# Performance work log

Hardware: AMD Instinct MI355X
Metric: run time of the kernel (lower is better)

## Reference

```python
import jax, jax.numpy as jnp
import numpy as np

CHUNK = 128
EPS = 1e-12


def causal_prod(q, k, v, chunk=CHUNK):
    """Chunk-parallel causal linear attention numerator and denominator.
    q,k: [B,H,S,D]; v: [B,H,S,E].
    Returns N: [B,H,S,E] = q_n . cumsum_{m<=n}(k_m v_m^T)
            D: [B,H,S]   = q_n . cumsum_{m<=n} k_m
    """
    B, H, S, D = q.shape
    E = v.shape[-1]
    nc = S // chunk
    # [nc, B, H, C, D]
    qc = q.reshape(B, H, nc, chunk, D).transpose(2, 0, 1, 3, 4)
    kc = k.reshape(B, H, nc, chunk, D).transpose(2, 0, 1, 3, 4)
    vc = v.reshape(B, H, nc, chunk, E).transpose(2, 0, 1, 3, 4)
    mask = jnp.tril(jnp.ones((chunk, chunk), dtype=bool))  # j <= i

    def step(carry, xs):
        S_state, Z_state = carry  # [B,H,D,E], [B,H,D]
        qb, kb, vb = xs           # [B,H,C,D], [B,H,C,D], [B,H,C,E]
        scores = jnp.einsum('bhid,bhjd->bhij', qb, kb)
        scores = jnp.where(mask, scores, 0.0)
        # intra-chunk causal part + inter-chunk state part
        Nb = jnp.einsum('bhij,bhje->bhie', scores, vb) \
             + jnp.einsum('bhid,bhde->bhie', qb, S_state)
        Db = scores.sum(-1) + jnp.einsum('bhid,bhd->bhi', qb, Z_state)
        S_state = S_state + jnp.einsum('bhjd,bhje->bhde', kb, vb)
        Z_state = Z_state + kb.sum(axis=2)
        return (S_state, Z_state), (Nb, Db)

    init = (jnp.zeros((B, H, D, E), q.dtype), jnp.zeros((B, H, D), q.dtype))
    _, (N, Dv) = jax.lax.scan(step, init, (qc, kc, vc))
    N = N.transpose(1, 2, 0, 3, 4).reshape(B, H, S, E)
    Dv = Dv.transpose(1, 2, 0, 3).reshape(B, H, S)
    return N, Dv


def setup_inputs() -> dict:
    key = jax.random.key(0)
    k0, k1, k2, k3, k4 = jax.random.split(key, 5)
    B, H, S, D = 2, 8, 4096, 64
    # feature-mapped q/k are positive (softmax random features) -> uniform
    q = jax.random.uniform(k0, (B, H, S, D), dtype=jnp.float32)
    k = jax.random.uniform(k1, (B, H, S, D), dtype=jnp.float32)
    q_rot = jax.random.uniform(k2, (B, H, S, D), dtype=jnp.float32)
    k_rot = jax.random.uniform(k3, (B, H, S, D), dtype=jnp.float32)
    v = jax.random.normal(k4, (B, H, S, D), dtype=jnp.float32)
    return {"q": q, "k": k, "q_rot": q_rot, "k_rot": k_rot, "v": v, "horizon": 512}


def reference(q, k, q_rot, k_rot, v, horizon):
    # causal_linear_attention with local=horizon, rotary branch active
    N1, D1 = causal_prod(q, k, v)
    N2, D2 = causal_prod(q_rot, k_rot, v)
    N = N1 + N2
    Dd = D1 + D2
    local = horizon
    # subtract contribution of keys older than the local window
    ql = q[:, :, local:]
    kl = k[:, :, :-local]
    vl = v[:, :, :-local]
    qrl = q_rot[:, :, local:]
    krl = k_rot[:, :, :-local]
    Ns1, Ds1 = causal_prod(ql, kl, vl)
    Ns2, Ds2 = causal_prod(qrl, krl, vl)
    N = N.at[:, :, local:].add(-(Ns1 + Ns2))
    Dd = Dd.at[:, :, local:].add(-(Ds1 + Ds2))
    out = N * (1.0 / (Dd + EPS))[..., None]
    return out
```

## Files before the change

kernel.cpp:

```cpp
#include <hip/hip_runtime.h>

#define S_LEN 4096
#define Dh 64
#define KC_TILE 16384
#define VT_TILE 8192

typedef __attribute__((ext_vector_type(8))) short bf16x8;
typedef __attribute__((ext_vector_type(4))) short bf16x4;
typedef __attribute__((ext_vector_type(4))) float f32x4;
typedef __attribute__((ext_vector_type(16))) float f32x16;
typedef __attribute__((ext_vector_type(4))) unsigned u32x4;

__device__ __forceinline__ short f2bf(float f) {
    union { float f; unsigned u; } c; c.f = f;
    unsigned u = c.u + 0x7FFFu + ((c.u >> 16) & 1u);
    return (short)(u >> 16);
}

__device__ __forceinline__ unsigned cvt_pk(float lo, float hi) {
    unsigned r;
    asm("v_cvt_pk_bf16_f32 %0, %1, %2" : "=v"(r) : "v"(lo), "v"(hi));
    return r;
}

__device__ __forceinline__ void pl32swap(unsigned& a, unsigned& b) {
    asm("v_permlane32_swap_b32 %0, %1" : "+v"(a), "+v"(b));
}

__global__ __launch_bounds__(256) void prepack3(
    const float* __restrict__ k, const float* __restrict__ kr,
    const float* __restrict__ v, char* __restrict__ ws,
    unsigned long long vt_base)
{
    const int bh = blockIdx.x >> 6;
    const int tile = blockIdx.x & 63;
    const int t = threadIdx.x;
    const size_t rowbase = ((size_t)bh * S_LEN + tile * 64) * Dh;

    __shared__ __align__(16) char sKc[16384];
    __shared__ __align__(16) char sVt[8192];

    #pragma unroll
    for (int i = 0; i < 4; ++i) {
        const int idx = t + 256 * i;
        const int f8 = idx & 15;
        const int key = idx >> 4;
        const int f0 = f8 * 8;
        const float* src = (f0 < 64) ? (k + rowbase + (size_t)key * Dh + f0)
                                     : (kr + rowbase + (size_t)key * Dh + (f0 - 64));
        f32x4 a = *(const f32x4*)src;
        f32x4 b = *(const f32x4*)(src + 4);
        u32x4 w;
        w[0] = cvt_pk(a[0], a[1]); w[1] = cvt_pk(a[2], a[3]);
        w[2] = cvt_pk(b[0], b[1]); w[3] = cvt_pk(b[2], b[3]);
        const int off = key * 256 + ((f0 * 2) ^ ((key & 7) << 4));
        *(u32x4*)(sKc + off) = w;
    }
    #pragma unroll
    for (int i = 0; i < 2; ++i) {
        const int idx = t + 256 * i;
        const int e8 = idx & 7;
        const int key = idx >> 3;
        const int e0 = e8 * 8;
        const float* src = v + rowbase + (size_t)key * Dh + e0;
        f32x4 a = *(const f32x4*)src;
        f32x4 b = *(const f32x4*)(src + 4);
        #pragma unroll
        for (int j = 0; j < 4; ++j) {
            int e = e0 + j;
            *(short*)(sVt + e * 128 + ((key * 2) ^ ((e & 7) << 4))) = f2bf(a[j]);
        }
        #pragma unroll
        for (int j = 0; j < 4; ++j) {
            int e = e0 + 4 + j;
            *(short*)(sVt + e * 128 + ((key * 2) ^ ((e & 7) << 4))) = f2bf(b[j]);
        }
    }
    __syncthreads();

    char* kdst = ws + (size_t)(bh * 64 + tile) * KC_TILE;
    #pragma unroll
    for (int i = 0; i < 4; ++i) {
        const int s = t + 256 * i;
        const int c = s >> 6;
        const int l = s & 63;
        const int fs = c >> 1, half = c & 1;
        const int key = half * 32 + (l & 31);
        const int f0 = fs * 16 + (l >> 5) * 8;
        const int off = key * 256 + ((f0 * 2) ^ ((key & 7) << 4));
        u32x4 w = *(const u32x4*)(sKc + off);
        *(u32x4*)(kdst + s * 16) = w;
    }
    char* vdst = ws + vt_base + (size_t)(bh * 64 + tile) * VT_TILE;
    #pragma unroll
    for (int i = 0; i < 2; ++i) {
        const int s = t + 256 * i;
        const int c = s >> 6;
        const int l = s & 63;
        const int kb = c >> 2, ks = (c >> 1) & 1, eh = c & 1;
        const int e = eh * 32 + (l & 31);
        const int key0 = kb * 32 + ks * 16 + (l >> 5) * 8;
        const int off = e * 128 + ((key0 * 2) ^ ((e & 7) << 4));
        u32x4 w = *(const u32x4*)(sVt + off);
        *(u32x4*)(vdst + s * 16) = w;
    }
}

__global__ __launch_bounds__(64, 2) void swin_attn8(
    const float* __restrict__ q, const float* __restrict__ qr,
    const char* __restrict__ ws, unsigned long long vt_base,
    const int* __restrict__ hor, float* __restrict__ out)
{
    const int W = hor[0];
    const int nwg = gridDim.x;
    const int cpx = nwg >> 3;
    const int bid = blockIdx.x;
    const int wg = (bid & 7) * cpx + (bid >> 3);
    const int bh = wg >> 7;
    const int q0 = (wg & 127) * 32;
    const size_t base = (size_t)bh * S_LEN * Dh;

    const int lane = threadIdx.x;
    const int hi = lane >> 5;
    const int l32 = lane & 31;

    __shared__ float sD[32];

    const int qg = q0 + l32;

    bf16x8 qf[8];
    {
        const float* qrow  = q  + base + (size_t)qg * Dh;
        const float* qrrow = qr + base + (size_t)qg * Dh;
        #pragma unroll
        for (int fs = 0; fs < 8; ++fs) {
            int feat = fs * 16 + hi * 8;
            const float* src = (feat < 64) ? (qrow + feat) : (qrrow + feat - 64);
            f32x4 a = *(const f32x4*)src;
            f32x4 b = *(const f32x4*)(src + 4);
            u32x4 w;
            w[0] = cvt_pk(a[0], a[1]); w[1] = cvt_pk(a[2], a[3]);
            w[2] = cvt_pk(b[0], b[1]); w[3] = cvt_pk(b[2], b[3]);
            qf[fs] = __builtin_bit_cast(bf16x8, w);
        }
    }

    f32x16 nacc0 = {};
    f32x16 nacc1 = {};
    float dsum = 0.f;

    const int lo_key = q0 - (W - 1);
    const int kt_lo = (lo_key <= 0) ? 0 : (lo_key >> 6);
    const int kt_hi = (q0 + 31) >> 6;

    const char* Kc = ws + (size_t)(bh << 6) * KC_TILE + lane * 16;
    const char* Vt = ws + vt_base + (size_t)(bh << 6) * VT_TILE + lane * 16;

    bf16x8 kf[16];
    bf16x8 vf[8];
    {
        const char* kp = Kc + (size_t)kt_lo * KC_TILE;
        const char* vp = Vt + (size_t)kt_lo * VT_TILE;
        #pragma unroll
        for (int c = 0; c < 16; ++c) kf[c] = *(const bf16x8*)(kp + c * 1024);
        #pragma unroll
        for (int c = 0; c < 8; ++c)  vf[c] = *(const bf16x8*)(vp + c * 1024);
    }

    for (int kt = kt_lo; kt <= kt_hi; ++kt) {
        const int k0 = kt << 6;
        const int ktn = (kt < kt_hi) ? kt + 1 : kt_hi;
        const bool dense = (k0 + 63 <= q0) && (k0 >= q0 + 32 - W);

        f32x16 sac0 = {};
        f32x16 sac1 = {};
        __builtin_amdgcn_s_setprio(1);
        #pragma unroll
        for (int fs = 0; fs < 8; ++fs) {
            sac0 = __builtin_amdgcn_mfma_f32_32x32x16_bf16(kf[fs * 2],     qf[fs], sac0, 0, 0, 0);
            sac1 = __builtin_amdgcn_mfma_f32_32x32x16_bf16(kf[fs * 2 + 1], qf[fs], sac1, 0, 0, 0);
        }
        __builtin_amdgcn_s_setprio(0);

        __builtin_amdgcn_sched_barrier(0);
        {
            const char* kp = Kc + (size_t)ktn * KC_TILE;
            #pragma unroll
            for (int c = 0; c < 16; ++c) kf[c] = *(const bf16x8*)(kp + c * 1024);
        }
        __builtin_amdgcn_sched_barrier(0);

        #pragma unroll
        for (int kb = 0; kb < 2; ++kb) {
            f32x16 s = kb ? sac1 : sac0;
            if (!dense) {
                #pragma unroll
                for (int r = 0; r < 16; ++r) {
                    int key = k0 + kb * 32 + (r & 3) + 8 * (r >> 2) + 4 * hi;
                    if ((unsigned)(qg - key) >= (unsigned)W) s[r] = 0.f;
                }
            }
            #pragma unroll
            for (int r = 0; r < 16; ++r) dsum += s[r];

            unsigned w0 = cvt_pk(s[0],  s[1]);
            unsigned w1 = cvt_pk(s[2],  s[3]);
            unsigned w2 = cvt_pk(s[4],  s[5]);
            unsigned w3 = cvt_pk(s[6],  s[7]);
            unsigned w4 = cvt_pk(s[8],  s[9]);
            unsigned w5 = cvt_pk(s[10], s[11]);
            unsigned w6 = cvt_pk(s[12], s[13]);
            unsigned w7 = cvt_pk(s[14], s[15]);
            pl32swap(w0, w2);
            pl32swap(w1, w3);
            pl32swap(w4, w6);
            pl32swap(w5, w7);
            u32x4 p0v = {w0, w1, w2, w3};
            u32x4 p1v = {w4, w5, w6, w7};
            bf16x8 pa0 = __builtin_bit_cast(bf16x8, p0v);
            bf16x8 pa1 = __builtin_bit_cast(bf16x8, p1v);

            __builtin_amdgcn_s_setprio(1);
            #pragma unroll
            for (int ks = 0; ks < 2; ++ks) {
                bf16x8 pa = ks ? pa1 : pa0;
                nacc0 = __builtin_amdgcn_mfma_f32_32x32x16_bf16(pa, vf[kb * 4 + ks * 2],     nacc0, 0, 0, 0);
                nacc1 = __builtin_amdgcn_mfma_f32_32x32x16_bf16(pa, vf[kb * 4 + ks * 2 + 1], nacc1, 0, 0, 0);
            }
            __builtin_amdgcn_s_setprio(0);
        }

        __builtin_amdgcn_sched_barrier(0);
        {
            const char* vp = Vt + (size_t)ktn * VT_TILE;
            #pragma unroll
            for (int c = 0; c < 8; ++c) vf[c] = *(const bf16x8*)(vp + c * 1024);
        }
        __builtin_amdgcn_sched_barrier(0);
    }

    unsigned da = __builtin_bit_cast(unsigned, dsum);
    unsigned db = da;
    pl32swap(da, db);
    float dfull = __builtin_bit_cast(float, da) + __builtin_bit_cast(float, db);
    float rcq = 1.0f / (dfull + 1e-12f);
    if (lane < 32) sD[l32] = rcq;
    __syncthreads();
    float rcv[16];
    #pragma unroll
    for (int r = 0; r < 16; ++r)
        rcv[r] = sD[(r & 3) + 8 * (r >> 2) + 4 * hi];

    #pragma unroll
    for (int r = 0; r < 16; ++r) {
        const int qrow = q0 + (r & 3) + 8 * (r >> 2) + 4 * hi;
        float* o = out + base + (size_t)qrow * Dh + l32;
        o[0]  = nacc0[r] * rcv[r];
        o[32] = nacc1[r] * rcv[r];
    }
}

__global__ __launch_bounds__(256, 2) void swin_attn_fb(
    const float* __restrict__ q, const float* __restrict__ k,
    const float* __restrict__ qr, const float* __restrict__ kr,
    const float* __restrict__ v, const int* __restrict__ hor,
    float* __restrict__ out)
{
    const int W = hor[0];
    const int q0 = blockIdx.x * 128;
    const int bh = blockIdx.y;
    const size_t base = (size_t)bh * S_LEN * Dh;

    const int tid = threadIdx.x;
    const int lane = tid & 63;
    const int wv = tid >> 6;
    const int g = lane >> 4;
    const int l16 = lane & 15;

    __shared__ __align__(16) char sK[64 * 256];
    __shared__ __align__(16) char sV[64 * 128];
    __shared__ __align__(16) char sS[4][32 * 128];

    bf16x8 qf[2][4];
    #pragma unroll
    for (int rb = 0; rb < 2; ++rb) {
        int qg = q0 + wv * 32 + rb * 16 + l16;
        const float* qrow  = q  + base + (size_t)qg * Dh;
        const float* qrrow = qr + base + (size_t)qg * Dh;
        #pragma unroll
        for (int fb = 0; fb < 4; ++fb) {
            int feat = fb * 32 + g * 8;
            const float* src = (feat < 64) ? (qrow + feat) : (qrrow + (feat - 64));
            f32x4 a = *(const f32x4*)src;
            f32x4 b = *(const f32x4*)(src + 4);
            bf16x8 fr;
            #pragma unroll
            for (int j = 0; j < 4; ++j) { fr[j] = f2bf(a[j]); fr[4 + j] = f2bf(b[j]); }
            qf[rb][fb] = fr;
        }
    }

    f32x4 nacc[2][4];
    f32x4 dacc[2];
    #pragma unroll
    for (int rb = 0; rb < 2; ++rb) {
        dacc[rb] = (f32x4){0.f, 0.f, 0.f, 0.f};
        #pragma unroll
        for (int eb = 0; eb < 4; ++eb) nacc[rb][eb] = (f32x4){0.f, 0.f, 0.f, 0.f};
    }
    bf16x8 ones;
    #pragma unroll
    for (int j = 0; j < 8; ++j) ones[j] = (short)0x3F80;

    const int lo_key = q0 - (W - 1);
    const int kt_lo = (lo_key <= 0) ? 0 : (lo_key >> 6);
    const int kt_hi = (q0 + 127) >> 6;

    for (int kt = kt_lo; kt <= kt_hi; ++kt) {
        const int k0 = kt << 6;
        __syncthreads();
        #pragma unroll
        for (int i = 0; i < 4; ++i) {
            int c = tid + 256 * i;
            int row = c >> 4;
            int f0 = (c & 15) * 8;
            const float* src = (f0 < 64) ? (k  + base + (size_t)(k0 + row) * Dh + f0)
                                         : (kr + base + (size_t)(k0 + row) * Dh + (f0 - 64));
            f32x4 a = *(const f32x4*)src;
            f32x4 b = *(const f32x4*)(src + 4);
            bf16x8 w8;
            #pragma unroll
            for (int j = 0; j < 4; ++j) { w8[j] = f2bf(a[j]); w8[4 + j] = f2bf(b[j]); }
            int off = row * 256 + ((f0 * 2) ^ ((row & 7) << 4));
            *(bf16x8*)(sK + off) = w8;
        }
        #pragma unroll
        for (int i = 0; i < 4; ++i) {
            int c = tid + 256 * i;
            int e = c & 63;
            int k4 = c >> 6;
            const float* src = v + base + (size_t)(k0 + k4 * 4) * Dh + e;
            bf16x4 w4;
            w4[0] = f2bf(src[0]); w4[1] = f2bf(src[Dh]);
            w4[2] = f2bf(src[2 * Dh]); w4[3] = f2bf(src[3 * Dh]);
            int off = e * 128 + ((k4 * 8) ^ ((e & 7) << 4));
            *(bf16x4*)(sV + off) = w4;
        }
        __syncthreads();

        const bool dense = (k0 + 63 <= q0) && (k0 >= q0 + 128 - W);
        #pragma unroll
        for (int kb = 0; kb < 4; ++kb) {
            bf16x8 kf[4];
            const int key = kb * 16 + l16;
            const int rowoff = key * 256;
            const int sw = (key & 7) << 4;
            #pragma unroll
            for (int fb = 0; fb < 4; ++fb)
                kf[fb] = *(const bf16x8*)(sK + rowoff + ((fb * 64 + g * 16) ^ sw));
            #pragma unroll
            for (int rb = 0; rb < 2; ++rb) {
                f32x4 s = {0.f, 0.f, 0.f, 0.f};
                #pragma unroll
                for (int fb = 0; fb < 4; ++fb)
                    s = __builtin_amdgcn_mfma_f32_16x16x32_bf16(qf[rb][fb], kf[fb], s, 0, 0, 0);
                const int qrow0 = rb * 16 + g * 4;
                const int qg0 = q0 + wv * 32 + qrow0;
                const int mg = k0 + kb * 16 + l16;
                if (!dense) {
                    #pragma unroll
                    for (int r = 0; r < 4; ++r) {
                        unsigned d = (unsigned)(qg0 + r - mg);
                        if (d >= (unsigned)W) s[r] = 0.f;
                    }
                }
                #pragma unroll
                for (int r = 0; r < 4; ++r) {
                    int row = qrow0 + r;
                    int off = row * 128 + (((kb * 16 + l16) * 2) ^ ((row & 7) << 4));
                    *(short*)(sS[wv] + off) = f2bf(s[r]);
                }
            }
        }
        #pragma unroll
        for (int kb2 = 0; kb2 < 2; ++kb2) {
            bf16x8 af[2];
            #pragma unroll
            for (int rb = 0; rb < 2; ++rb) {
                int row = rb * 16 + l16;
                int off = row * 128 + ((kb2 * 64 + g * 16) ^ ((row & 7) << 4));
                af[rb] = *(const bf16x8*)(sS[wv] + off);
            }
            #pragma unroll
            for (int rb = 0; rb < 2; ++rb)
                dacc[rb] = __builtin_amdgcn_mfma_f32_16x16x32_bf16(af[rb], ones, dacc[rb], 0, 0, 0);
            #pragma unroll
            for (int eb = 0; eb < 4; ++eb) {
                int e = eb * 16 + l16;
                int off = e * 128 + ((kb2 * 64 + g * 16) ^ ((e & 7) << 4));
                bf16x8 bfr = *(const bf16x8*)(sV + off);
                #pragma unroll
                for (int rb = 0; rb < 2; ++rb)
                    nacc[rb][eb] = __builtin_amdgcn_mfma_f32_16x16x32_bf16(af[rb], bfr, nacc[rb][eb], 0, 0, 0);
            }
        }
    }

    #pragma unroll
    for (int rb = 0; rb < 2; ++rb) {
        f32x4 rc;
        #pragma unroll
        for (int r = 0; r < 4; ++r) rc[r] = 1.0f / (dacc[rb][r] + 1e-12f);
        const int qg0 = q0 + wv * 32 + rb * 16 + g * 4;
        #pragma unroll
        for (int eb = 0; eb < 4; ++eb) {
            #pragma unroll
            for (int r = 0; r < 4; ++r) {
                out[base + (size_t)(qg0 + r) * Dh + eb * 16 + l16] = nacc[rb][eb][r] * rc[r];
            }
        }
    }
}

extern "C" void kernel_launch(void* const* d_in, const int* in_sizes, int n_in,
                              void* d_out, int out_size, void* d_ws, size_t ws_size,
                              hipStream_t stream) {
    const float* q  = (const float*)d_in[0];
    const float* k  = (const float*)d_in[1];
    const float* qr = (const float*)d_in[2];
    const float* kr = (const float*)d_in[3];
    const float* v  = (const float*)d_in[4];
    const int* hor  = (const int*)d_in[5];
    float* out = (float*)d_out;

    const int BH = in_sizes[0] / (S_LEN * Dh);
    const unsigned long long vt_base = (unsigned long long)BH * 64 * KC_TILE;
    const unsigned long long ws_need = (unsigned long long)BH * 64 * (KC_TILE + VT_TILE);

    if (ws_size >= ws_need) {
        hipLaunchKernelGGL(prepack3, dim3(BH * 64), dim3(256), 0, stream,
                           k, kr, v, (char*)d_ws, vt_base);
        hipLaunchKernelGGL(swin_attn8, dim3(BH * 128), dim3(64), 0, stream,
                           q, qr, (const char*)d_ws, vt_base, hor, out);
    } else {
        hipLaunchKernelGGL(swin_attn_fb, dim3(S_LEN / 128, BH), dim3(256), 0, stream,
                           q, k, qr, kr, v, hor, out);
    }
}
```

Before: 43.21 us.

## Share K/V tiles across four waves via LDS double-buffered async loads

The attention kernel now runs four waves per workgroup covering 128 query rows. Each K/V tile is staged once into LDS with global_load_lds, double-buffered, and all four waves read it. Before, every 32-row wave fetched its own K/V fragments from global memory into registers. This cuts redundant global/L2 traffic and register pressure, at the cost of per-tile barriers, LDS reads, and some extra tiles computed at window edges because the key range is set per workgroup.

```diff
diff --git a/kernel.cpp b/kernel.cpp
--- a/kernel.cpp
+++ b/kernel.cpp
@@ -25,6 +25,12 @@
 
 __device__ __forceinline__ void pl32swap(unsigned& a, unsigned& b) {
     asm("v_permlane32_swap_b32 %0, %1" : "+v"(a), "+v"(b));
+}
+
+__device__ __forceinline__ void gload16(const void* g, void* l) {
+    __builtin_amdgcn_global_load_lds(
+        (const __attribute__((address_space(1))) unsigned int*)g,
+        (__attribute__((address_space(3))) unsigned int*)l, 16, 0, 0);
 }
 
 __global__ __launch_bounds__(256) void prepack3(
@@ -106,7 +112,7 @@
     }
 }
 
-__global__ __launch_bounds__(64, 2) void swin_attn8(
+__global__ __launch_bounds__(256, 2) void swin_attn9(
     const float* __restrict__ q, const float* __restrict__ qr,
     const char* __restrict__ ws, unsigned long long vt_base,
     const int* __restrict__ hor, float* __restrict__ out)
@@ -116,17 +122,22 @@
     const int cpx = nwg >> 3;
     const int bid = blockIdx.x;
     const int wg = (bid & 7) * cpx + (bid >> 3);
-    const int bh = wg >> 7;
-    const int q0 = (wg & 127) * 32;
+    const int bh = wg >> 5;
+    const int q0 = (wg & 31) * 128;
     const size_t base = (size_t)bh * S_LEN * Dh;
 
-    const int lane = threadIdx.x;
+    const int tid = threadIdx.x;
+    const int lane = tid & 63;
+    const int wv = tid >> 6;
     const int hi = lane >> 5;
     const int l32 = lane & 31;
 
-    __shared__ float sD[32];
-
-    const int qg = q0 + l32;
+    __shared__ __align__(16) char sK[2][KC_TILE];
+    __shared__ __align__(16) char sV[2][VT_TILE];
+    __shared__ float sD[4][32];
+
+    const int q0w = q0 + wv * 32;
+    const int qg = q0w + l32;
 
     bf16x8 qf[8];
     {
@@ -151,44 +162,56 @@
 
     const int lo_key = q0 - (W - 1);
     const int kt_lo = (lo_key <= 0) ? 0 : (lo_key >> 6);
-    const int kt_hi = (q0 + 31) >> 6;
-
-    const char* Kc = ws + (size_t)(bh << 6) * KC_TILE + lane * 16;
-    const char* Vt = ws + vt_base + (size_t)(bh << 6) * VT_TILE + lane * 16;
-
-    bf16x8 kf[16];
-    bf16x8 vf[8];
-    {
-        const char* kp = Kc + (size_t)kt_lo * KC_TILE;
-        const char* vp = Vt + (size_t)kt_lo * VT_TILE;
-        #pragma unroll
-        for (int c = 0; c < 16; ++c) kf[c] = *(const bf16x8*)(kp + c * 1024);
-        #pragma unroll
-        for (int c = 0; c < 8; ++c)  vf[c] = *(const bf16x8*)(vp + c * 1024);
-    }
-
+    const int kt_hi = (q0 + 127) >> 6;
+
+    const char* KcB = ws + (size_t)(bh << 6) * KC_TILE;
+    const char* VtB = ws + vt_base + (size_t)(bh << 6) * VT_TILE;
+
+    asm volatile("s_waitcnt vmcnt(0)" ::: "memory");
+    __builtin_amdgcn_sched_barrier(0);
+
+#define STAGE(B, KT)                                                              \
+    do {                                                                          \
+        const char* kg_ = KcB + (size_t)(KT) * KC_TILE + wv * 4096 + lane * 16;   \
+        const char* vg_ = VtB + (size_t)(KT) * VT_TILE + wv * 2048 + lane * 16;   \
+        _Pragma("unroll")                                                         \
+        for (int i_ = 0; i_ < 4; ++i_)                                            \
+            gload16(kg_ + i_ * 1024, &sK[B][wv * 4096 + i_ * 1024]);              \
+        _Pragma("unroll")                                                         \
+        for (int i_ = 0; i_ < 2; ++i_)                                            \
+            gload16(vg_ + i_ * 1024, &sV[B][wv * 2048 + i_ * 1024]);              \
+    } while (0)
+
+    STAGE(0, kt_lo);
+
+    int buf = 0;
     for (int kt = kt_lo; kt <= kt_hi; ++kt) {
         const int k0 = kt << 6;
-        const int ktn = (kt < kt_hi) ? kt + 1 : kt_hi;
-        const bool dense = (k0 + 63 <= q0) && (k0 >= q0 + 32 - W);
+        if (kt < kt_hi) {
+            STAGE(buf ^ 1, kt + 1);
+            asm volatile("s_waitcnt vmcnt(6)" ::: "memory");
+        } else {
+            asm volatile("s_waitcnt vmcnt(0)" ::: "memory");
+        }
+        __builtin_amdgcn_sched_barrier(0);
+        __builtin_amdgcn_s_barrier();
+        asm volatile("" ::: "memory");
+
+        const char* Kb = sK[buf];
+        const char* Vb = sV[buf];
+        const bool dense = (k0 + 63 <= q0w) && (k0 >= q0w + 32 - W);
 
         f32x16 sac0 = {};
         f32x16 sac1 = {};
         __builtin_amdgcn_s_setprio(1);
         #pragma unroll
         for (int fs = 0; fs < 8; ++fs) {
-            sac0 = __builtin_amdgcn_mfma_f32_32x32x16_bf16(kf[fs * 2],     qf[fs], sac0, 0, 0, 0);
-            sac1 = __builtin_amdgcn_mfma_f32_32x32x16_bf16(kf[fs * 2 + 1], qf[fs], sac1, 0, 0, 0);
+            bf16x8 kf0 = *(const bf16x8*)(Kb + (fs * 2) * 1024 + lane * 16);
+            bf16x8 kf1 = *(const bf16x8*)(Kb + (fs * 2 + 1) * 1024 + lane * 16);
+            sac0 = __builtin_amdgcn_mfma_f32_32x32x16_bf16(kf0, qf[fs], sac0, 0, 0, 0);
+            sac1 = __builtin_amdgcn_mfma_f32_32x32x16_bf16(kf1, qf[fs], sac1, 0, 0, 0);
         }
         __builtin_amdgcn_s_setprio(0);
-
-        __builtin_amdgcn_sched_barrier(0);
-        {
-            const char* kp = Kc + (size_t)ktn * KC_TILE;
-            #pragma unroll
-            for (int c = 0; c < 16; ++c) kf[c] = *(const bf16x8*)(kp + c * 1024);
-        }
-        __builtin_amdgcn_sched_barrier(0);
 
         #pragma unroll
         for (int kb = 0; kb < 2; ++kb) {
@@ -224,36 +247,35 @@
             #pragma unroll
             for (int ks = 0; ks < 2; ++ks) {
                 bf16x8 pa = ks ? pa1 : pa0;
-                nacc0 = __builtin_amdgcn_mfma_f32_32x32x16_bf16(pa, vf[kb * 4 + ks * 2],     nacc0, 0, 0, 0);
-                nacc1 = __builtin_amdgcn_mfma_f32_32x32x16_bf16(pa, vf[kb * 4 + ks * 2 + 1], nacc1, 0, 0, 0);
+                bf16x8 vf0 = *(const bf16x8*)(Vb + (kb * 4 + ks * 2) * 1024 + lane * 16);
+                bf16x8 vf1 = *(const bf16x8*)(Vb + (kb * 4 + ks * 2 + 1) * 1024 + lane * 16);
+                nacc0 = __builtin_amdgcn_mfma_f32_32x32x16_bf16(pa, vf0, nacc0, 0, 0, 0);
+                nacc1 = __builtin_amdgcn_mfma_f32_32x32x16_bf16(pa, vf1, nacc1, 0, 0, 0);
             }
             __builtin_amdgcn_s_setprio(0);
         }
 
-        __builtin_amdgcn_sched_barrier(0);
-        {
-            const char* vp = Vt + (size_t)ktn * VT_TILE;
-            #pragma unroll
-            for (int c = 0; c < 8; ++c) vf[c] = *(const bf16x8*)(vp + c * 1024);
-        }
-        __builtin_amdgcn_sched_barrier(0);
-    }
+        asm volatile("" ::: "memory");
+        __builtin_amdgcn_s_barrier();
+        buf ^= 1;
+    }
+#undef STAGE
 
     unsigned da = __builtin_bit_cast(unsigned, dsum);
     unsigned db = da;
     pl32swap(da, db);
     float dfull = __builtin_bit_cast(float, da) + __builtin_bit_cast(float, db);
     float rcq = 1.0f / (dfull + 1e-12f);
-    if (lane < 32) sD[l32] = rcq;
+    if (lane < 32) sD[wv][l32] = rcq;
     __syncthreads();
     float rcv[16];
     #pragma unroll
     for (int r = 0; r < 16; ++r)
-        rcv[r] = sD[(r & 3) + 8 * (r >> 2) + 4 * hi];
+        rcv[r] = sD[wv][(r & 3) + 8 * (r >> 2) + 4 * hi];
 
     #pragma unroll
     for (int r = 0; r < 16; ++r) {
-        const int qrow = q0 + (r & 3) + 8 * (r >> 2) + 4 * hi;
+        const int qrow = q0w + (r & 3) + 8 * (r >> 2) + 4 * hi;
         float* o = out + base + (size_t)qrow * Dh + l32;
         o[0]  = nacc0[r] * rcv[r];
         o[32] = nacc1[r] * rcv[r];
@@ -440,7 +462,7 @@
     if (ws_size >= ws_need) {
         hipLaunchKernelGGL(prepack3, dim3(BH * 64), dim3(256), 0, stream,
                            k, kr, v, (char*)d_ws, vt_base);
-        hipLaunchKernelGGL(swin_attn8, dim3(BH * 128), dim3(64), 0, stream,
+        hipLaunchKernelGGL(swin_attn9, dim3(BH * 32), dim3(256), 0, stream,
                            q, qr, (const char*)d_ws, vt_base, hor, out);
     } else {
         hipLaunchKernelGGL(swin_attn_fb, dim3(S_LEN / 128, BH), dim3(256), 0, stream,
```

After: 41.12 us. 1.05x faster.
